# Performance work log

Hardware: AMD Instinct MI355X
Metric: run time of the kernel (lower is better)

The kernel has to match this reference:

```python
import jax, jax.numpy as jnp
import numpy as np

ANCHORS = np.array([[10,13],[16,30],[33,23],[30,61],[62,45],[59,119],
                    [116,90],[156,198],[373,326]], dtype=np.float32)
MASKS = [[6,7,8],[3,4,5],[0,1,2]]
NUM_CLASSES = 80
INPUT = 416.0          # input_shape == image_shape (no letterbox correction needed)
CONF_THRES = 0.5
NMS_THRES = 0.3
TOPK = 300             # fixed candidate budget per image (pad/mask for jit)


def decode_level(feat, mask):
    """feat: [B, A*(5+C), H, W] -> [B, A*H*W, 5+C] normalized xywh+conf+cls."""
    B, _, H, W = feat.shape
    A = len(mask)
    t = feat.reshape(B, A, 5 + NUM_CLASSES, H, W).transpose(0, 1, 3, 4, 2)  # [B,A,H,W,85]
    gy, gx = jnp.meshgrid(jnp.arange(H, dtype=feat.dtype),
                          jnp.arange(W, dtype=feat.dtype), indexing='ij')
    anc = jnp.asarray(ANCHORS[np.array(mask)])                    # [A,2] in input pixels
    x = (jax.nn.sigmoid(t[..., 0]) + gx) / W
    y = (jax.nn.sigmoid(t[..., 1]) + gy) / H
    w = jnp.exp(t[..., 2]) * anc[:, 0][None, :, None, None] / INPUT
    h = jnp.exp(t[..., 3]) * anc[:, 1][None, :, None, None] / INPUT
    conf = jax.nn.sigmoid(t[..., 4])
    cls = jax.nn.sigmoid(t[..., 5:])
    out = jnp.concatenate([jnp.stack([x, y, w, h, conf], axis=-1), cls], axis=-1)
    return out.reshape(B, A * H * W, 5 + NUM_CLASSES)


def pairwise_iou(b):
    # b: [K,4] corner boxes
    area = (b[:, 2] - b[:, 0]) * (b[:, 3] - b[:, 1])
    lt = jnp.maximum(b[:, None, :2], b[None, :, :2])
    rb = jnp.minimum(b[:, None, 2:], b[None, :, 2:])
    wh = jnp.clip(rb - lt, 0.0)
    inter = wh[..., 0] * wh[..., 1]
    return inter / (area[:, None] + area[None, :] - inter + 1e-6)


def nms_image(pred):
    """pred: [N, 5+C] -> [TOPK, 6] = (x1,y1,x2,y2,score,class), zero-padded."""
    obj = pred[:, 4]
    cls_conf = jnp.max(pred[:, 5:], axis=-1)
    cls_id = jnp.argmax(pred[:, 5:], axis=-1)
    score = obj * cls_conf
    score = jnp.where(score >= CONF_THRES, score, 0.0)   # confidence filter (masked)
    score_top, idx = jax.lax.top_k(score, TOPK)
    xywh = pred[idx, :4]
    boxes = jnp.concatenate([xywh[:, :2] - xywh[:, 2:] * 0.5,
                             xywh[:, :2] + xywh[:, 2:] * 0.5], axis=-1) * INPUT
    cls_top = cls_id[idx]
    # class-aware NMS via coordinate offset trick
    off = cls_top.astype(boxes.dtype)[:, None] * (2.0 * INPUT)
    iou = pairwise_iou(boxes + off)
    ar = jnp.arange(TOPK)

    def body(i, keep):
        sup = (iou[i] > NMS_THRES) & (ar > i) & keep[i]
        return keep & ~sup

    keep = jax.lax.fori_loop(0, TOPK, body, jnp.ones(TOPK, dtype=bool))
    valid = keep & (score_top > 0.0)
    m = valid.astype(boxes.dtype)
    return jnp.concatenate([boxes * m[:, None],
                            (score_top * m)[:, None],
                            (cls_top.astype(boxes.dtype) * m)[:, None]], axis=-1)


def setup_inputs() -> dict:
    key = jax.random.key(0)
    k0, k1, k2 = jax.random.split(key, 3)
    B, C = 32, 3 * (5 + NUM_CLASSES)
    return {
        'feat0': jax.random.normal(k0, (B, C, 13, 13), dtype=jnp.float32),
        'feat1': jax.random.normal(k1, (B, C, 26, 26), dtype=jnp.float32),
        'feat2': jax.random.normal(k2, (B, C, 52, 52), dtype=jnp.float32),
    }


def reference(feat0, feat1, feat2):
    outputs = jnp.concatenate([
        decode_level(feat0, MASKS[0]),
        decode_level(feat1, MASKS[1]),
        decode_level(feat2, MASKS[2]),
    ], axis=1)                      # [B, 10647, 85]
    return jax.vmap(nms_image)(outputs)   # [B, TOPK, 6]
```

## Files before the change

kernel.cpp:

```cpp
#include <hip/hip_runtime.h>
#include <math.h>

#define NUM_CLASSES 80
#define TOPK 300
#define NTOT 10647
#define L0END 507
#define L1END 2535
#define CTR_STRIDE 64
#define SELCAP 2048

__constant__ float ANCWf[3][3] = {{116.f,156.f,373.f},{30.f,62.f,59.f},{10.f,16.f,33.f}};
__constant__ float ANCHf[3][3] = {{90.f,198.f,326.f},{61.f,45.f,119.f},{13.f,30.f,23.f}};

__device__ __forceinline__ float expcr(float x) { return (float)exp((double)x); }
__device__ __forceinline__ float sigf(float x) {
    float e = expcr(-x);
    return __fdiv_rn(1.0f, __fadd_rn(1.0f, e));
}

__device__ __forceinline__ const float* locate(const float* f0, const float* f1, const float* f2,
                                               int img, int idx,
                                               int& level, int& hw, int& W, int& hrow, int& wcol, int& a) {
    int local, cell;
    const float* base;
    if (idx < L0END) {
        level = 0; local = idx; hw = 169; W = 13;
        base = f0 + (size_t)img * 43095;
    } else if (idx < L1END) {
        level = 1; local = idx - L0END; hw = 676; W = 26;
        base = f1 + (size_t)img * 172380;
    } else {
        level = 2; local = idx - L1END; hw = 2704; W = 52;
        base = f2 + (size_t)img * 689520;
    }
    a = local / hw; cell = local - a * hw;
    hrow = cell / W; wcol = cell - hrow * W;
    return base + (size_t)(a * 85) * hw + cell;
}

__global__ void score_kernel(const float* __restrict__ f0, const float* __restrict__ f1,
                             const float* __restrict__ f2,
                             unsigned int* __restrict__ counters,
                             unsigned long long* __restrict__ keys) {
    int t = blockIdx.x * blockDim.x + threadIdx.x;
    int lane = threadIdx.x & 63;

    bool pred[4] = {false, false, false, false};
    unsigned int kidx[4];
    float kscore[4];
    int img;

    if (t < 32 * 512) {
        img = t >> 9;
        int r = t & 511;
        if (r < 507) {
            int a = r / 169, cell = r - a * 169;
            const float* p = f0 + (size_t)img * 43095 + (size_t)(a * 85) * 169 + cell;
            float obj = sigf(p[4 * 169]);
            float mx = p[5 * 169];
            #pragma unroll 8
            for (int c = 1; c < NUM_CLASSES; ++c) {
                float v = p[(5 + c) * 169];
                if (v > mx) mx = v;
            }
            float s = __fmul_rn(obj, sigf(mx));
            if (s >= 0.5f) { pred[0] = true; kidx[0] = r; kscore[0] = s; }
        }
    } else if (t < 64 * 512) {
        int tt = t - 32 * 512;
        img = tt >> 9;
        int r = tt & 511;
        if (r < 507) {
            int a = r / 169, grp = r - a * 169;
            int cell0 = grp * 4;
            const float* p0 = f1 + (size_t)img * 172380 + (size_t)(a * 85) * 676 + cell0;
            float4 o4 = *(const float4*)(p0 + 4 * 676);
            float4 mx = *(const float4*)(p0 + 5 * 676);
            #pragma unroll 8
            for (int c = 1; c < NUM_CLASSES; ++c) {
                float4 v = *(const float4*)(p0 + (5 + c) * 676);
                mx.x = fmaxf(mx.x, v.x); mx.y = fmaxf(mx.y, v.y);
                mx.z = fmaxf(mx.z, v.z); mx.w = fmaxf(mx.w, v.w);
            }
            float ob[4] = {o4.x, o4.y, o4.z, o4.w};
            float mv[4] = {mx.x, mx.y, mx.z, mx.w};
            #pragma unroll
            for (int j = 0; j < 4; ++j) {
                float s = __fmul_rn(sigf(ob[j]), sigf(mv[j]));
                if (s >= 0.5f) { pred[j] = true; kidx[j] = L0END + a * 676 + cell0 + j; kscore[j] = s; }
            }
        }
    } else {
        int tt = t - 64 * 512;
        img = tt >> 11;
        int r = tt & 2047;
        if (r < 2028) {
            int a = r / 676, grp = r - a * 676;
            int cell0 = grp * 4;
            const float* p0 = f2 + (size_t)img * 689520 + (size_t)(a * 85) * 2704 + cell0;
            float4 o4 = *(const float4*)(p0 + 4 * 2704);
            float4 mx = *(const float4*)(p0 + 5 * 2704);
            #pragma unroll 8
            for (int c = 1; c < NUM_CLASSES; ++c) {
                float4 v = *(const float4*)(p0 + (5 + c) * 2704);
                mx.x = fmaxf(mx.x, v.x); mx.y = fmaxf(mx.y, v.y);
                mx.z = fmaxf(mx.z, v.z); mx.w = fmaxf(mx.w, v.w);
            }
            float ob[4] = {o4.x, o4.y, o4.z, o4.w};
            float mv[4] = {mx.x, mx.y, mx.z, mx.w};
            #pragma unroll
            for (int j = 0; j < 4; ++j) {
                float s = __fmul_rn(sigf(ob[j]), sigf(mv[j]));
                if (s >= 0.5f) { pred[j] = true; kidx[j] = L1END + a * 2704 + cell0 + j; kscore[j] = s; }
            }
        }
    }

    unsigned long long* kout = keys + (size_t)img * NTOT;
    unsigned int* ctr = &counters[img * CTR_STRIDE];
    #pragma unroll
    for (int j = 0; j < 4; ++j) {
        unsigned long long mask = __ballot(pred[j]);
        if (mask) {
            int lead = __ffsll((long long)mask) - 1;
            unsigned int base = 0;
            if (lane == lead) base = atomicAdd(ctr, (unsigned int)__popcll(mask));
            base = __shfl(base, lead, 64);
            if (pred[j]) {
                unsigned int pos = (unsigned int)__popcll(mask & ((1ULL << lane) - 1ULL));
                kout[base + pos] = ((unsigned long long)__float_as_uint(kscore[j]) << 32)
                                   | (unsigned int)(~kidx[j]);
            }
        }
    }
}

__global__ __launch_bounds__(1024) void topk_kernel(const unsigned int* __restrict__ counters,
                                                    const unsigned long long* __restrict__ keys,
                                                    unsigned int* __restrict__ top_idx) {
    __shared__ unsigned int hist[1024];
    __shared__ unsigned int scan[1024];
    __shared__ unsigned long long sel[SELCAP];
    __shared__ unsigned int cnt;
    __shared__ int Tbin;

    int img = blockIdx.x;
    int tid = threadIdx.x;
    int n = (int)counters[img * CTR_STRIDE];
    if (n > NTOT) n = NTOT;
    const unsigned long long* k = keys + (size_t)img * NTOT;

    hist[tid] = 0;
    if (tid == 0) { cnt = 0; Tbin = 0; }
    for (int i = tid; i < TOPK; i += 1024) top_idx[img * TOPK + i] = 0xFFFFFFFFu;
    __syncthreads();

    for (int i = tid; i < n; i += 1024) {
        unsigned int sb = (unsigned int)(k[i] >> 32);
        int bin = (int)((sb - 0x3F000000u) >> 13);
        if (bin > 1023) bin = 1023;
        atomicAdd(&hist[bin], 1u);
    }
    __syncthreads();

    scan[tid] = hist[tid];
    __syncthreads();
    for (int off = 1; off < 1024; off <<= 1) {
        unsigned int v = (tid + off < 1024) ? scan[tid + off] : 0u;
        __syncthreads();
        scan[tid] += v;
        __syncthreads();
    }
    {
        unsigned int snext = (tid < 1023) ? scan[tid + 1] : 0u;
        if (scan[tid] >= TOPK && snext < TOPK) Tbin = tid;
    }
    __syncthreads();
    int T = Tbin;

    for (int i = tid; i < n; i += 1024) {
        unsigned long long kv = k[i];
        unsigned int sb = (unsigned int)(kv >> 32);
        int bin = (int)((sb - 0x3F000000u) >> 13);
        if (bin > 1023) bin = 1023;
        if (bin >= T) {
            unsigned int pos = atomicAdd(&cnt, 1u);
            if (pos < SELCAP) sel[pos] = kv;
        }
    }
    __syncthreads();
    int m = (int)cnt; if (m > SELCAP) m = SELCAP;

    for (int i = tid; i < m; i += 1024) {
        unsigned long long ki = sel[i];
        int rank = 0;
        for (int j = 0; j < m; ++j) rank += (sel[j] > ki);
        if (rank < TOPK) top_idx[img * TOPK + rank] = ~((unsigned int)ki);
    }
}

__global__ __launch_bounds__(256) void decode_top_kernel(const float* __restrict__ f0,
                                                         const float* __restrict__ f1,
                                                         const float* __restrict__ f2,
                                                         const unsigned int* __restrict__ top_idx,
                                                         float* __restrict__ rows, int nrows) {
    int gw = blockIdx.x * 4 + (threadIdx.x >> 6);
    int lane = threadIdx.x & 63;
    if (gw >= nrows) return;
    int img = gw / TOPK, k = gw - img * TOPK;
    float* row = rows + (size_t)gw * 8;
    unsigned int idx = top_idx[img * TOPK + k];
    if (idx == 0xFFFFFFFFu) {
        if (lane < 8) row[lane] = 0.0f;
        return;
    }
    int level, hw, W, hrow, wcol, a;
    const float* p = locate(f0, f1, f2, img, (int)idx, level, hw, W, hrow, wcol, a);

    float v1 = p[(5 + lane) * hw];
    float bestv = sigf(v1);
    int besti = lane;
    if (lane < 16) {
        float v2 = p[(69 + lane) * hw];
        float sv2 = sigf(v2);
        if (sv2 > bestv) { bestv = sv2; besti = 64 + lane; }
    }
    #pragma unroll
    for (int off = 32; off > 0; off >>= 1) {
        float ov = __shfl_xor(bestv, off, 64);
        int oi = __shfl_xor(besti, off, 64);
        if (ov > bestv || (ov == bestv && oi < besti)) { bestv = ov; besti = oi; }
    }

    float tval = (lane < 5) ? p[lane * hw] : 0.0f;
    float tx = __shfl(tval, 0, 64);
    float ty = __shfl(tval, 1, 64);
    float tw = __shfl(tval, 2, 64);
    float th = __shfl(tval, 3, 64);
    float tob = __shfl(tval, 4, 64);

    if (lane == 0) {
        float x = __fdiv_rn(__fadd_rn(sigf(tx), (float)wcol), (float)W);
        float y = __fdiv_rn(__fadd_rn(sigf(ty), (float)hrow), (float)W);
        float wd = __fdiv_rn(__fmul_rn(expcr(tw), ANCWf[level][a]), 416.0f);
        float ht = __fdiv_rn(__fmul_rn(expcr(th), ANCHf[level][a]), 416.0f);
        float obj = sigf(tob);
        float score = __fmul_rn(obj, bestv);
        if (!(score >= 0.5f)) score = 0.0f;

        float hx = __fmul_rn(wd, 0.5f);
        float hy = __fmul_rn(ht, 0.5f);
        float x1 = __fmul_rn(__fsub_rn(x, hx), 416.0f);
        float y1 = __fmul_rn(__fsub_rn(y, hy), 416.0f);
        float x2 = __fmul_rn(__fadd_rn(x, hx), 416.0f);
        float y2 = __fmul_rn(__fadd_rn(y, hy), 416.0f);

        row[0] = x1; row[1] = y1; row[2] = x2; row[3] = y2;
        row[4] = score; row[5] = (float)besti; row[6] = 0.0f; row[7] = 0.0f;
    }
}

__global__ __launch_bounds__(512) void nms_core_kernel(const float* __restrict__ rows,
                                                       float* __restrict__ out) {
    __shared__ float bx0[TOPK], bx1[TOPK], bx2[TOPK], bx3[TOPK];
    __shared__ float bb0[TOPK], bb1[TOPK], bb2[TOPK], bb3[TOPK];
    __shared__ float area[TOPK], sc[TOPK], clsf[TOPK];
    __shared__ unsigned long long sup[TOPK][5];
    __shared__ unsigned long long keepm[5];

    int img = blockIdx.x;
    int tid = threadIdx.x;
    int wave = tid >> 6, lane = tid & 63;

    if (tid < TOPK) {
        const float* row = rows + ((size_t)img * TOPK + tid) * 8;
        float x1 = row[0], y1 = row[1], x2 = row[2], y2 = row[3];
        float score = row[4], cf = row[5];
        float off = __fmul_rn(cf, 832.0f);
        bx0[tid] = x1; bx1[tid] = y1; bx2[tid] = x2; bx3[tid] = y2;
        float b0 = __fadd_rn(x1, off), b1 = __fadd_rn(y1, off);
        float b2 = __fadd_rn(x2, off), b3 = __fadd_rn(y2, off);
        bb0[tid] = b0; bb1[tid] = b1; bb2[tid] = b2; bb3[tid] = b3;
        area[tid] = __fmul_rn(__fsub_rn(b2, b0), __fsub_rn(b3, b1));
        sc[tid] = score;
        clsf[tid] = cf;
    }
    __syncthreads();

    for (int r = wave; r < TOPK; r += 8) {
        float a0 = bb0[r], a1 = bb1[r], a2 = bb2[r], a3 = bb3[r], aa = area[r];
        #pragma unroll
        for (int w = 0; w < 5; ++w) {
            int j = (w << 6) + lane;
            bool bit = false;
            if (j > r && j < TOPK) {
                float ltx = fmaxf(a0, bb0[j]);
                float lty = fmaxf(a1, bb1[j]);
                float rbx = fminf(a2, bb2[j]);
                float rby = fminf(a3, bb3[j]);
                float wx = fmaxf(__fsub_rn(rbx, ltx), 0.0f);
                float wy = fmaxf(__fsub_rn(rby, lty), 0.0f);
                float inter = __fmul_rn(wx, wy);
                float denom = __fadd_rn(__fsub_rn(__fadd_rn(aa, area[j]), inter), 1e-6f);
                float iou = __fdiv_rn(inter, denom);
                bit = (iou > 0.3f);
            }
            unsigned long long m = __ballot(bit);
            if (lane == 0) sup[r][w] = m;
        }
    }
    __syncthreads();

    if (wave == 0) {
        unsigned long long srow[5][5];
        #pragma unroll
        for (int s = 0; s < 5; ++s) {
            int r = (s << 6) + lane;
            #pragma unroll
            for (int w = 0; w < 5; ++w)
                srow[s][w] = (r < TOPK) ? sup[r][w] : 0ULL;
        }
        unsigned long long kp[5] = {~0ULL, ~0ULL, ~0ULL, ~0ULL, ~0ULL};
        #pragma unroll
        for (int s = 0; s < 5; ++s) {
            int nii = (s == 4) ? (TOPK - 256) : 64;
            for (int ii = 0; ii < nii; ++ii) {
                unsigned long long r0 = __shfl(srow[s][0], ii, 64);
                unsigned long long r1 = __shfl(srow[s][1], ii, 64);
                unsigned long long r2 = __shfl(srow[s][2], ii, 64);
                unsigned long long r3 = __shfl(srow[s][3], ii, 64);
                unsigned long long r4 = __shfl(srow[s][4], ii, 64);
                if ((kp[s] >> ii) & 1ULL) {
                    kp[0] &= ~r0; kp[1] &= ~r1; kp[2] &= ~r2; kp[3] &= ~r3; kp[4] &= ~r4;
                }
            }
        }
        if (lane == 0) {
            keepm[0] = kp[0]; keepm[1] = kp[1]; keepm[2] = kp[2];
            keepm[3] = kp[3]; keepm[4] = kp[4];
        }
    }
    __syncthreads();

    if (tid < TOPK) {
        bool kept = (keepm[tid >> 6] >> (tid & 63)) & 1ULL;
        float m = (kept && (sc[tid] > 0.0f)) ? 1.0f : 0.0f;
        float* o = out + ((size_t)img * TOPK + tid) * 6;
        o[0] = __fmul_rn(bx0[tid], m);
        o[1] = __fmul_rn(bx1[tid], m);
        o[2] = __fmul_rn(bx2[tid], m);
        o[3] = __fmul_rn(bx3[tid], m);
        o[4] = __fmul_rn(sc[tid], m);
        o[5] = __fmul_rn(clsf[tid], m);
    }
}

extern "C" void kernel_launch(void* const* d_in, const int* in_sizes, int n_in,
                              void* d_out, int out_size, void* d_ws, size_t ws_size,
                              hipStream_t stream) {
    const float* f0 = (const float*)d_in[0];
    const float* f1 = (const float*)d_in[1];
    const float* f2 = (const float*)d_in[2];
    float* out = (float*)d_out;

    int B = in_sizes[0] / 43095;
    int nrows = B * TOPK;

    unsigned int* counters = (unsigned int*)d_ws;
    size_t off1 = (size_t)B * CTR_STRIDE * sizeof(unsigned int);
    unsigned int* top_idx = (unsigned int*)((char*)d_ws + off1);
    size_t off2 = off1 + ((size_t)nrows * sizeof(unsigned int) + 255) / 256 * 256;
    float* rows = (float*)((char*)d_ws + off2);
    size_t off3 = off2 + ((size_t)nrows * 8 * sizeof(float) + 255) / 256 * 256;
    unsigned long long* keys = (unsigned long long*)((char*)d_ws + off3);

    hipMemsetAsync(counters, 0, off1, stream);
    score_kernel<<<98304 / 256, 256, 0, stream>>>(f0, f1, f2, counters, keys);
    topk_kernel<<<B, 1024, 0, stream>>>(counters, keys, top_idx);
    decode_top_kernel<<<(nrows + 3) / 4, 256, 0, stream>>>(f0, f1, f2, top_idx, rows, nrows);
    nms_core_kernel<<<B, 512, 0, stream>>>(rows, out);
}
```

Measured before the change: 118.3 us.

## Widen NMS block, hoist per-lane box loads, simplify greedy keep sweep

Doubles the NMS kernel block to 1024 threads so more waves compute IoU suppression rows in parallel. It swaps the loop order so each lane keeps its column box in registers across rows. It replaces the register-heavy greedy suppression loop with a single-word-per-lane sweep that broadcasts the keep bit via shuffle and reads suppression rows from shared memory. This trades fewer registers and fewer shuffles for a shared-memory read per iteration in the serial loop.

Result: faster. 104.6 us (-11.6%).

```diff
diff --git a/kernel.cpp b/kernel.cpp
--- a/kernel.cpp
+++ b/kernel.cpp
@@ -260,8 +260,8 @@
     }
 }
 
-__global__ __launch_bounds__(512) void nms_core_kernel(const float* __restrict__ rows,
-                                                       float* __restrict__ out) {
+__global__ __launch_bounds__(1024) void nms_core_kernel(const float* __restrict__ rows,
+                                                        float* __restrict__ out) {
     __shared__ float bx0[TOPK], bx1[TOPK], bx2[TOPK], bx3[TOPK];
     __shared__ float bb0[TOPK], bb1[TOPK], bb2[TOPK], bb3[TOPK];
     __shared__ float area[TOPK], sc[TOPK], clsf[TOPK];
@@ -287,21 +287,27 @@
     }
     __syncthreads();
 
-    for (int r = wave; r < TOPK; r += 8) {
-        float a0 = bb0[r], a1 = bb1[r], a2 = bb2[r], a3 = bb3[r], aa = area[r];
-        #pragma unroll
-        for (int w = 0; w < 5; ++w) {
-            int j = (w << 6) + lane;
+    #pragma unroll
+    for (int w = 0; w < 5; ++w) {
+        int j = (w << 6) + lane;
+        bool jv = (j < TOPK);
+        float j0 = jv ? bb0[j] : 0.0f;
+        float j1 = jv ? bb1[j] : 0.0f;
+        float j2 = jv ? bb2[j] : 0.0f;
+        float j3 = jv ? bb3[j] : 0.0f;
+        float ja = jv ? area[j] : 0.0f;
+        for (int r = wave; r < TOPK; r += 16) {
+            float a0 = bb0[r], a1 = bb1[r], a2 = bb2[r], a3 = bb3[r], aa = area[r];
             bool bit = false;
-            if (j > r && j < TOPK) {
-                float ltx = fmaxf(a0, bb0[j]);
-                float lty = fmaxf(a1, bb1[j]);
-                float rbx = fminf(a2, bb2[j]);
-                float rby = fminf(a3, bb3[j]);
+            if (jv && j > r) {
+                float ltx = fmaxf(a0, j0);
+                float lty = fmaxf(a1, j1);
+                float rbx = fminf(a2, j2);
+                float rby = fminf(a3, j3);
                 float wx = fmaxf(__fsub_rn(rbx, ltx), 0.0f);
                 float wy = fmaxf(__fsub_rn(rby, lty), 0.0f);
                 float inter = __fmul_rn(wx, wy);
-                float denom = __fadd_rn(__fsub_rn(__fadd_rn(aa, area[j]), inter), 1e-6f);
+                float denom = __fadd_rn(__fsub_rn(__fadd_rn(aa, ja), inter), 1e-6f);
                 float iou = __fdiv_rn(inter, denom);
                 bit = (iou > 0.3f);
             }
@@ -312,33 +318,13 @@
     __syncthreads();
 
     if (wave == 0) {
-        unsigned long long srow[5][5];
-        #pragma unroll
-        for (int s = 0; s < 5; ++s) {
-            int r = (s << 6) + lane;
-            #pragma unroll
-            for (int w = 0; w < 5; ++w)
-                srow[s][w] = (r < TOPK) ? sup[r][w] : 0ULL;
-        }
-        unsigned long long kp[5] = {~0ULL, ~0ULL, ~0ULL, ~0ULL, ~0ULL};
-        #pragma unroll
-        for (int s = 0; s < 5; ++s) {
-            int nii = (s == 4) ? (TOPK - 256) : 64;
-            for (int ii = 0; ii < nii; ++ii) {
-                unsigned long long r0 = __shfl(srow[s][0], ii, 64);
-                unsigned long long r1 = __shfl(srow[s][1], ii, 64);
-                unsigned long long r2 = __shfl(srow[s][2], ii, 64);
-                unsigned long long r3 = __shfl(srow[s][3], ii, 64);
-                unsigned long long r4 = __shfl(srow[s][4], ii, 64);
-                if ((kp[s] >> ii) & 1ULL) {
-                    kp[0] &= ~r0; kp[1] &= ~r1; kp[2] &= ~r2; kp[3] &= ~r3; kp[4] &= ~r4;
-                }
-            }
-        }
-        if (lane == 0) {
-            keepm[0] = kp[0]; keepm[1] = kp[1]; keepm[2] = kp[2];
-            keepm[3] = kp[3]; keepm[4] = kp[4];
-        }
+        unsigned long long kp = ~0ULL;
+        for (int i = 0; i < TOPK; ++i) {
+            unsigned long long kw = __shfl(kp, i >> 6, 64);
+            bool keep_i = (kw >> (i & 63)) & 1ULL;
+            if (keep_i && lane < 5) kp &= ~sup[i][lane];
+        }
+        if (lane < 5) keepm[lane] = kp;
     }
     __syncthreads();
 
@@ -378,5 +364,5 @@
     score_kernel<<<98304 / 256, 256, 0, stream>>>(f0, f1, f2, counters, keys);
     topk_kernel<<<B, 1024, 0, stream>>>(counters, keys, top_idx);
     decode_top_kernel<<<(nrows + 3) / 4, 256, 0, stream>>>(f0, f1, f2, top_idx, rows, nrows);
-    nms_core_kernel<<<B, 512, 0, stream>>>(rows, out);
-}
+    nms_core_kernel<<<B, 1024, 0, stream>>>(rows, out);
+}
```
